# Kernel tuning notes

Hardware: AMD Instinct MI355X
Metric: run time of the kernel (lower is better)

Reference implementation:

```python
import jax, jax.numpy as jnp
import numpy as np
from jax import lax

DN = ('NCDHW', 'OIDHW', 'NCDHW')


def _ln(x, w, b, eps=1e-5):
    m = jnp.mean(x, -1, keepdims=True)
    v = jnp.mean((x - m) ** 2, -1, keepdims=True)
    return (x - m) * lax.rsqrt(v + eps) * w + b


def _gelu(x):
    return jax.nn.gelu(x, approximate=False)


def _dwconv3(v, w, b, groups):
    # depthwise 3x3x3, padding=1, stride=1; v:[B,C,H,W,D], w:[C,1,3,3,3]
    y = lax.conv_general_dilated(v, w, (1, 1, 1), 'SAME',
                                 dimension_numbers=DN,
                                 feature_group_count=groups)
    return y + b[None, :, None, None, None]


def _forward(x, ln1_w, ln1_b, q_w, sr1_w, sr1_b, n1_w, n1_b, sr2_w, sr2_b,
             n2_w, n2_b, kv1_w, kv2_w, lc1_w, lc1_b, lc2_w, lc2_b,
             proj_w, proj_b, ln2_w, ln2_b, fc1_w, fc1_b, fc2_w, fc2_b,
             H, W, D):
    B, N, C = x.shape
    h = 8
    h2 = h // 2
    hd = C // h
    scale = hd ** -0.5
    C2 = C // 2

    # ---- pre-norm + attention ----
    xa = _ln(x, ln1_w, ln1_b)
    q = (xa @ q_w.T).reshape(B, N, h, hd).transpose(0, 2, 1, 3)  # [B,h,N,hd]

    x_ = xa.transpose(0, 2, 1).reshape(B, C, H, W, D)
    # branch 1: conv k=2 s=2 spatial reduction
    y1 = lax.conv_general_dilated(x_, sr1_w, (2, 2, 2), 'VALID',
                                  dimension_numbers=DN) + sr1_b[None, :, None, None, None]
    N1 = (H // 2) * (W // 2) * (D // 2)
    x1 = _gelu(_ln(y1.reshape(B, C, N1).transpose(0, 2, 1), n1_w, n1_b))  # [B,N1,C]
    # branch 2: 1x1x1 conv, full resolution
    y2 = lax.conv_general_dilated(x_, sr2_w, (1, 1, 1), 'VALID',
                                  dimension_numbers=DN) + sr2_b[None, :, None, None, None]
    N2 = N
    x2 = _gelu(_ln(y2.reshape(B, C, N2).transpose(0, 2, 1), n2_w, n2_b))  # [B,N2,C]

    kv1 = (x1 @ kv1_w.T).reshape(B, N1, 2, h2, hd).transpose(2, 0, 3, 1, 4)
    k1, v1 = kv1[0], kv1[1]  # [B,h2,N1,hd]
    kv2 = (x2 @ kv2_w.T).reshape(B, N2, 2, h2, hd).transpose(2, 0, 3, 1, 4)
    k2, v2 = kv2[0], kv2[1]  # [B,h2,N2,hd]

    attn1 = jax.nn.softmax(jnp.einsum('bhnd,bhmd->bhnm', q[:, :h2], k1) * scale, axis=-1)
    v1sp = v1.transpose(0, 2, 1, 3).reshape(B, N1, C2).transpose(0, 2, 1).reshape(
        B, C2, H // 2, W // 2, D // 2)
    v1 = v1 + _dwconv3(v1sp, lc1_w, lc1_b, C2).reshape(B, h2, hd, N1).transpose(0, 1, 3, 2)
    o1 = jnp.einsum('bhnm,bhmd->bhnd', attn1, v1).transpose(0, 2, 1, 3).reshape(B, N, C2)

    attn2 = jax.nn.softmax(jnp.einsum('bhnd,bhmd->bhnm', q[:, h2:], k2) * scale, axis=-1)
    v2sp = v2.transpose(0, 2, 1, 3).reshape(B, N2, C2).transpose(0, 2, 1).reshape(B, C2, H, W, D)
    v2 = v2 + _dwconv3(v2sp, lc2_w, lc2_b, C2).reshape(B, h2, hd, N2).transpose(0, 1, 3, 2)
    o2 = jnp.einsum('bhnm,bhmd->bhnd', attn2, v2).transpose(0, 2, 1, 3).reshape(B, N, C2)

    att = jnp.concatenate([o1, o2], axis=-1) @ proj_w.T + proj_b
    x = x + att  # residual (drop_path = 0)

    # ---- pre-norm + MLP ----
    xm = _ln(x, ln2_w, ln2_b)
    mlp = _gelu(xm @ fc1_w.T + fc1_b) @ fc2_w.T + fc2_b
    return x + mlp


def setup_inputs() -> dict:
    key = jax.random.key(0)
    B, C, H, W, D = 2, 384, 16, 16, 16
    N = H * W * D
    hid = 4 * C
    C2 = C // 2
    ks = iter(jax.random.split(key, 32))
    rn = lambda shape, s=0.02: (jax.random.normal(next(ks), shape) * s).astype(jnp.float32)
    return {
        'x': jax.random.normal(next(ks), (B, N, C), jnp.float32),
        'ln1_w': jnp.ones(C, jnp.float32), 'ln1_b': jnp.zeros(C, jnp.float32),
        'q_w': rn((C, C)),
        'sr1_w': rn((C, C, 2, 2, 2), 0.025), 'sr1_b': jnp.zeros(C, jnp.float32),
        'n1_w': jnp.ones(C, jnp.float32), 'n1_b': jnp.zeros(C, jnp.float32),
        'sr2_w': rn((C, C, 1, 1, 1), 0.07), 'sr2_b': jnp.zeros(C, jnp.float32),
        'n2_w': jnp.ones(C, jnp.float32), 'n2_b': jnp.zeros(C, jnp.float32),
        'kv1_w': rn((C, C)), 'kv2_w': rn((C, C)),
        'lc1_w': rn((C2, 1, 3, 3, 3), 0.27), 'lc1_b': jnp.zeros(C2, jnp.float32),
        'lc2_w': rn((C2, 1, 3, 3, 3), 0.27), 'lc2_b': jnp.zeros(C2, jnp.float32),
        'proj_w': rn((C, C)), 'proj_b': jnp.zeros(C, jnp.float32),
        'ln2_w': jnp.ones(C, jnp.float32), 'ln2_b': jnp.zeros(C, jnp.float32),
        'fc1_w': rn((hid, C)), 'fc1_b': jnp.zeros(hid, jnp.float32),
        'fc2_w': rn((C, hid)), 'fc2_b': jnp.zeros(C, jnp.float32),
        'H': H, 'W': W, 'D': D,
    }


def reference(x, ln1_w, ln1_b, q_w, sr1_w, sr1_b, n1_w, n1_b, sr2_w, sr2_b,
              n2_w, n2_b, kv1_w, kv2_w, lc1_w, lc1_b, lc2_w, lc2_b,
              proj_w, proj_b, ln2_w, ln2_b, fc1_w, fc1_b, fc2_w, fc2_b,
              H, W, D):
    return _forward(x, ln1_w, ln1_b, q_w, sr1_w, sr1_b, n1_w, n1_b, sr2_w, sr2_b,
                    n2_w, n2_b, kv1_w, kv2_w, lc1_w, lc1_b, lc2_w, lc2_b,
                    proj_w, proj_b, ln2_w, ln2_b, fc1_w, fc1_b, fc2_w, fc2_b,
                    H, W, D)
```

## Files before the change

kernel.cpp:

```cpp
#include <hip/hip_runtime.h>

typedef unsigned short ushort_t;
typedef unsigned int uint_t;
typedef __bf16 bf16_t;
typedef __bf16 bf16x8 __attribute__((ext_vector_type(8)));
typedef float f32x4 __attribute__((ext_vector_type(4)));

__device__ __forceinline__ float b2f(ushort_t u) {
    union { uint_t i; float f; } v; v.i = ((uint_t)u) << 16; return v.f;
}
__device__ __forceinline__ ushort_t f2b(float f) {
    union { float f; uint_t i; } v; v.f = f;
    uint_t r = v.i + 0x7fffu + ((v.i >> 16) & 1u);
    return (ushort_t)(r >> 16);
}
__device__ __forceinline__ float gelu_exact(float x) {
    return 0.5f * x * (1.0f + erff(x * 0.70710678118654752f));
}

__global__ void prep_weights(const float* __restrict__ q_w, const float* __restrict__ sr2_w,
                             const float* __restrict__ kv1_w, const float* __restrict__ kv2_w,
                             const float* __restrict__ proj_w, const float* __restrict__ fc1_w,
                             const float* __restrict__ fc2_w, const float* __restrict__ sr1_w,
                             ushort_t* __restrict__ dst) {
    int gid = blockIdx.x * 256 + threadIdx.x;
    int i = gid;
    if (i < 147456) { dst[gid] = f2b(q_w[i]); return; }
    i -= 147456;
    if (i < 147456) { dst[gid] = f2b(sr2_w[i]); return; }
    i -= 147456;
    if (i < 147456) { dst[gid] = f2b(kv1_w[i]); return; }
    i -= 147456;
    if (i < 147456) { dst[gid] = f2b(kv2_w[i]); return; }
    i -= 147456;
    if (i < 147456) { dst[gid] = f2b(proj_w[i]); return; }
    i -= 147456;
    if (i < 589824) { dst[gid] = f2b(fc1_w[i]); return; }
    i -= 589824;
    if (i < 589824) { dst[gid] = f2b(fc2_w[i]); return; }
    i -= 589824;
    if (i < 1179648) {
        int co = i / 3072, r = i % 3072, kk = r / 384, ci = r % 384;
        dst[gid] = f2b(sr1_w[((size_t)co * 384 + ci) * 8 + kk]);
    }
}

__global__ void im2col_kernel(const ushort_t* __restrict__ xa, ushort_t* __restrict__ A1) {
    int gid = blockIdx.x * 256 + threadIdx.x;
    if (gid >= 1024 * 3072) return;
    int m = gid / 3072, r = gid % 3072, kk = r / 384, ci = r % 384;
    int b = m >> 9, n1 = m & 511;
    int ho = n1 >> 6, wo = (n1 >> 3) & 7, dz = n1 & 7;
    int n = ((2 * ho + ((kk >> 2) & 1)) << 8) + ((2 * wo + ((kk >> 1) & 1)) << 4) + (2 * dz + (kk & 1));
    A1[gid] = xa[((size_t)b * 4096 + n) * 384 + ci];
}

__global__ __launch_bounds__(128) void ln_kernel(const float* __restrict__ in,
                                                 const float* __restrict__ w,
                                                 const float* __restrict__ b,
                                                 float* __restrict__ outf,
                                                 ushort_t* __restrict__ outb, int act) {
    const int C = 384;
    int row = blockIdx.x, tid = threadIdx.x;
    size_t base = (size_t)row * C;
    float x[3], s = 0.f, s2 = 0.f;
#pragma unroll
    for (int i = 0; i < 3; i++) {
        int c = tid + i * 128;
        float v = in[base + c];
        x[i] = v; s += v; s2 += v * v;
    }
    for (int off = 32; off; off >>= 1) { s += __shfl_down(s, off); s2 += __shfl_down(s2, off); }
    __shared__ float sc[4];
    int lane = tid & 63, wid = tid >> 6;
    if (lane == 0) { sc[wid] = s; sc[wid + 2] = s2; }
    __syncthreads();
    float ts = sc[0] + sc[1], ts2 = sc[2] + sc[3];
    float mean = ts / C;
    float var = ts2 / C - mean * mean;
    float rstd = rsqrtf(var + 1e-5f);
#pragma unroll
    for (int i = 0; i < 3; i++) {
        int c = tid + i * 128;
        float v = (x[i] - mean) * rstd * w[c] + b[c];
        if (act) v = gelu_exact(v);
        if (outf) outf[base + c] = v;
        if (outb) outb[base + c] = f2b(v);
    }
}

__global__ __launch_bounds__(256) void mfma_gemm(const ushort_t* __restrict__ A,
                                                 const ushort_t* __restrict__ W,
                                                 const float* __restrict__ bias,
                                                 const float* __restrict__ res,
                                                 float* __restrict__ outf,
                                                 ushort_t* __restrict__ outb,
                                                 int M, int N, int K, int act) {
    __shared__ bf16_t Asl[128][40];
    __shared__ bf16_t Wsl[128][40];
    int tid = threadIdx.x;
    int wave = tid >> 6, lane = tid & 63, g = lane >> 4, c = lane & 15;
    int wm = wave >> 1, wn = wave & 1;
    int m0 = blockIdx.y * 128, n0 = blockIdx.x * 128;
    int srow = tid >> 1, sseg = tid & 1;

    f32x4 acc[4][4];
#pragma unroll
    for (int i = 0; i < 4; i++)
#pragma unroll
        for (int j = 0; j < 4; j++) acc[i][j] = f32x4{0.f, 0.f, 0.f, 0.f};

    for (int k0 = 0; k0 < K; k0 += 32) {
        const ushort_t* As = A + (size_t)(m0 + srow) * K + k0 + sseg * 16;
        const ushort_t* Ws = W + (size_t)(n0 + srow) * K + k0 + sseg * 16;
        uint4 av0 = *(const uint4*)As, av1 = *(const uint4*)(As + 8);
        uint4 wv0 = *(const uint4*)Ws, wv1 = *(const uint4*)(Ws + 8);
        __syncthreads();
        *(uint4*)&Asl[srow][sseg * 16] = av0;
        *(uint4*)&Asl[srow][sseg * 16 + 8] = av1;
        *(uint4*)&Wsl[srow][sseg * 16] = wv0;
        *(uint4*)&Wsl[srow][sseg * 16 + 8] = wv1;
        __syncthreads();
        bf16x8 af[4], bf[4];
#pragma unroll
        for (int fi = 0; fi < 4; fi++) af[fi] = *(bf16x8*)&Asl[wm * 64 + fi * 16 + c][g * 8];
#pragma unroll
        for (int fj = 0; fj < 4; fj++) bf[fj] = *(bf16x8*)&Wsl[wn * 64 + fj * 16 + c][g * 8];
#pragma unroll
        for (int fi = 0; fi < 4; fi++)
#pragma unroll
            for (int fj = 0; fj < 4; fj++)
                acc[fi][fj] = __builtin_amdgcn_mfma_f32_16x16x32_bf16(af[fi], bf[fj], acc[fi][fj], 0, 0, 0);
    }

#pragma unroll
    for (int fi = 0; fi < 4; fi++) {
#pragma unroll
        for (int fj = 0; fj < 4; fj++) {
            int n = n0 + wn * 64 + fj * 16 + c;
            float bv = bias ? bias[n] : 0.f;
#pragma unroll
            for (int i = 0; i < 4; i++) {
                int m = m0 + wm * 64 + fi * 16 + 4 * g + i;
                float v = acc[fi][fj][i] + bv;
                if (act == 1) v = gelu_exact(v);
                size_t idx = (size_t)m * N + n;
                if (res) v += res[idx];
                if (outf) outf[idx] = v;
                if (outb) outb[idx] = f2b(v);
            }
        }
    }
}

__global__ __launch_bounds__(256) void gemm64(const ushort_t* __restrict__ A,
                                              const ushort_t* __restrict__ W,
                                              const float* __restrict__ bias,
                                              const float* __restrict__ res,
                                              float* __restrict__ outf,
                                              ushort_t* __restrict__ outb,
                                              int M, int N, int K, int act, float oscale) {
    __shared__ bf16_t Asl[64][72];
    __shared__ bf16_t Wsl[64][72];
    int tid = threadIdx.x;
    int wave = tid >> 6, lane = tid & 63, g = lane >> 4, c = lane & 15;
    int wm = wave >> 1, wn = wave & 1;
    int m0 = blockIdx.y * 64, n0 = blockIdx.x * 64;
    int srow = tid >> 2, sseg = tid & 3;

    f32x4 acc[2][2];
#pragma unroll
    for (int i = 0; i < 2; i++)
#pragma unroll
        for (int j = 0; j < 2; j++) acc[i][j] = f32x4{0.f, 0.f, 0.f, 0.f};

    for (int k0 = 0; k0 < K; k0 += 64) {
        const ushort_t* As = A + (size_t)(m0 + srow) * K + k0 + sseg * 16;
        const ushort_t* Ws = W + (size_t)(n0 + srow) * K + k0 + sseg * 16;
        uint4 av0 = *(const uint4*)As, av1 = *(const uint4*)(As + 8);
        uint4 wv0 = *(const uint4*)Ws, wv1 = *(const uint4*)(Ws + 8);
        __syncthreads();
        *(uint4*)&Asl[srow][sseg * 16] = av0;
        *(uint4*)&Asl[srow][sseg * 16 + 8] = av1;
        *(uint4*)&Wsl[srow][sseg * 16] = wv0;
        *(uint4*)&Wsl[srow][sseg * 16 + 8] = wv1;
        __syncthreads();
#pragma unroll
        for (int kk = 0; kk < 2; kk++) {
            bf16x8 af[2], bf[2];
#pragma unroll
            for (int fi = 0; fi < 2; fi++) af[fi] = *(bf16x8*)&Asl[wm * 32 + fi * 16 + c][kk * 32 + g * 8];
#pragma unroll
            for (int fj = 0; fj < 2; fj++) bf[fj] = *(bf16x8*)&Wsl[wn * 32 + fj * 16 + c][kk * 32 + g * 8];
#pragma unroll
            for (int fi = 0; fi < 2; fi++)
#pragma unroll
                for (int fj = 0; fj < 2; fj++)
                    acc[fi][fj] = __builtin_amdgcn_mfma_f32_16x16x32_bf16(af[fi], bf[fj], acc[fi][fj], 0, 0, 0);
        }
    }

#pragma unroll
    for (int fi = 0; fi < 2; fi++) {
#pragma unroll
        for (int fj = 0; fj < 2; fj++) {
            int n = n0 + wn * 32 + fj * 16 + c;
            float bv = bias ? bias[n] : 0.f;
#pragma unroll
            for (int i = 0; i < 4; i++) {
                int m = m0 + wm * 32 + fi * 16 + 4 * g + i;
                float v = (acc[fi][fj][i] + bv) * oscale;
                if (act == 1) v = gelu_exact(v);
                size_t idx = (size_t)m * N + n;
                if (res) v += res[idx];
                if (outf) outf[idx] = v;
                if (outb) outb[idx] = f2b(v);
            }
        }
    }
}

__global__ __launch_bounds__(256) void gemm_qy2(const ushort_t* __restrict__ A,
                                                const ushort_t* __restrict__ W,
                                                const float* __restrict__ sr2_b,
                                                ushort_t* __restrict__ qb,
                                                float* __restrict__ y2f,
                                                int M, float qscale) {
    const int K = 384;
    __shared__ bf16_t Asl[64][72];
    __shared__ bf16_t Wsl[64][72];
    int tid = threadIdx.x;
    int wave = tid >> 6, lane = tid & 63, g = lane >> 4, c = lane & 15;
    int wm = wave >> 1, wn = wave & 1;
    int m0 = blockIdx.y * 64, n0 = blockIdx.x * 64;
    int srow = tid >> 2, sseg = tid & 3;

    f32x4 acc[2][2];
#pragma unroll
    for (int i = 0; i < 2; i++)
#pragma unroll
        for (int j = 0; j < 2; j++) acc[i][j] = f32x4{0.f, 0.f, 0.f, 0.f};

    for (int k0 = 0; k0 < K; k0 += 64) {
        const ushort_t* As = A + (size_t)(m0 + srow) * K + k0 + sseg * 16;
        const ushort_t* Ws = W + (size_t)(n0 + srow) * K + k0 + sseg * 16;
        uint4 av0 = *(const uint4*)As, av1 = *(const uint4*)(As + 8);
        uint4 wv0 = *(const uint4*)Ws, wv1 = *(const uint4*)(Ws + 8);
        __syncthreads();
        *(uint4*)&Asl[srow][sseg * 16] = av0;
        *(uint4*)&Asl[srow][sseg * 16 + 8] = av1;
        *(uint4*)&Wsl[srow][sseg * 16] = wv0;
        *(uint4*)&Wsl[srow][sseg * 16 + 8] = wv1;
        __syncthreads();
#pragma unroll
        for (int kk = 0; kk < 2; kk++) {
            bf16x8 af[2], bf[2];
#pragma unroll
            for (int fi = 0; fi < 2; fi++) af[fi] = *(bf16x8*)&Asl[wm * 32 + fi * 16 + c][kk * 32 + g * 8];
#pragma unroll
            for (int fj = 0; fj < 2; fj++) bf[fj] = *(bf16x8*)&Wsl[wn * 32 + fj * 16 + c][kk * 32 + g * 8];
#pragma unroll
            for (int fi = 0; fi < 2; fi++)
#pragma unroll
                for (int fj = 0; fj < 2; fj++)
                    acc[fi][fj] = __builtin_amdgcn_mfma_f32_16x16x32_bf16(af[fi], bf[fj], acc[fi][fj], 0, 0, 0);
        }
    }

    int isq = (n0 < 384);
#pragma unroll
    for (int fi = 0; fi < 2; fi++) {
#pragma unroll
        for (int fj = 0; fj < 2; fj++) {
            int n = n0 + wn * 32 + fj * 16 + c;
#pragma unroll
            for (int i = 0; i < 4; i++) {
                int m = m0 + wm * 32 + fi * 16 + 4 * g + i;
                float v = acc[fi][fj][i];
                if (isq) {
                    qb[(size_t)m * 384 + n] = f2b(v * qscale);
                } else {
                    y2f[(size_t)m * 384 + (n - 384)] = v + sr2_b[n - 384];
                }
            }
        }
    }
}

__global__ void dwconv_kernel(const ushort_t* __restrict__ vin,
                              const float* __restrict__ wt,
                              const float* __restrict__ bias,
                              ushort_t* __restrict__ vout,
                              int Hs, int Wsz, int Ds, int S, int total) {
    int gid = blockIdx.x * 256 + threadIdx.x;
    if (gid >= total) return;
    int c2 = gid % 192;
    int r = gid / 192;
    int n = r % S;
    int b = r / S;
    int dz = n % Ds, wy = (n / Ds) % Wsz, hx = n / (Wsz * Ds);
    float center = b2f(vin[(size_t)(b * S + n) * 384 + c2]);
    float acc = bias[c2];
    for (int kh = -1; kh <= 1; kh++) {
        int h2 = hx + kh; if (h2 < 0 || h2 >= Hs) continue;
        for (int kw = -1; kw <= 1; kw++) {
            int w2 = wy + kw; if (w2 < 0 || w2 >= Wsz) continue;
            for (int kd = -1; kd <= 1; kd++) {
                int d2 = dz + kd; if (d2 < 0 || d2 >= Ds) continue;
                int nn = (h2 * Wsz + w2) * Ds + d2;
                acc += b2f(vin[(size_t)(b * S + nn) * 384 + c2]) *
                       wt[c2 * 27 + (kh + 1) * 9 + (kw + 1) * 3 + (kd + 1)];
            }
        }
    }
    vout[(size_t)(b * S + n) * 192 + c2] = f2b(center + acc);
}

__global__ __launch_bounds__(256) void transpose_kernel(const ushort_t* __restrict__ src,
                                                        ushort_t* __restrict__ dst, int S) {
    __shared__ ushort_t t_lds[64][65];
    int n0 = blockIdx.x * 64, c0 = blockIdx.y * 64, b = blockIdx.z;
    int tid = threadIdx.x;
#pragma unroll
    for (int i = 0; i < 16; i++) {
        int idx = tid + i * 256;
        int r = idx >> 6, cc = idx & 63;
        t_lds[r][cc] = src[((size_t)b * S + n0 + r) * 192 + c0 + cc];
    }
    __syncthreads();
#pragma unroll
    for (int i = 0; i < 16; i++) {
        int idx = tid + i * 256;
        int r = idx >> 6, cc = idx & 63;
        dst[((size_t)b * 192 + c0 + r) * S + n0 + cc] = t_lds[cc][r];
    }
}

__global__ __launch_bounds__(256, 4) void attn_mfma5(
    const ushort_t* __restrict__ qbuf,
    const ushort_t* __restrict__ kv1,
    const ushort_t* __restrict__ kv2,
    const ushort_t* __restrict__ vt1,
    const ushort_t* __restrict__ vt2,
    ushort_t* __restrict__ obuf)
{
    __shared__ __align__(16) char lds_raw[18432];
    bf16_t (*P)[32][72] = (bf16_t (*)[32][72])lds_raw;
    float (*CF)[64][14] = (float (*)[64][14])lds_raw;

    const int N = 4096;
    int tid = threadIdx.x;
    int q0 = blockIdx.x * 32, hl = 7 - blockIdx.y, b = blockIdx.z;
    int wave = tid >> 6, lane = tid & 63, g = lane >> 4, c = lane & 15;
    int br2 = hl >> 2;
    int NK = br2 ? 4096 : 512;
    const ushort_t* kbuf = br2 ? kv2 : kv1;
    const ushort_t* vtb  = br2 ? vt2 : vt1;
    int hloc = hl & 3;
    int NKc = NK >> 2;
    int kb0 = wave * NKc;
    int nkt = NKc >> 6;

    union { uint4 u; bf16x8 v; } zz; zz.u = uint4{0u, 0u, 0u, 0u};
    const bf16x8 zero8 = zz.v;

    bf16x8 bq0[2], bq1[2];
#pragma unroll
    for (int qg = 0; qg < 2; qg++) {
        const ushort_t* qrowp = qbuf + ((size_t)b * N + q0 + qg * 16 + c) * 384 + hl * 48;
        bq0[qg] = *(const bf16x8*)(qrowp + g * 8);
        bq1[qg] = (g < 2) ? *(const bf16x8*)(qrowp + 32 + g * 8) : zero8;
    }

    f32x4 of[3][2];
#pragma unroll
    for (int dt = 0; dt < 3; dt++)
#pragma unroll
        for (int qg = 0; qg < 2; qg++) of[dt][qg] = f32x4{0.f, 0.f, 0.f, 0.f};
    float l_acc[2] = {0.f, 0.f};

    const ushort_t* kp = kbuf + ((size_t)b * NK + kb0 + c) * 384 + hloc * 48;
    const ushort_t* vp = vtb + ((size_t)b * 192 + hloc * 48 + c) * NK + kb0;

    for (int kt = 0; kt < nkt; kt++) {
        f32x4 sf[4][2];
#pragma unroll
        for (int t = 0; t < 4; t++)
#pragma unroll
            for (int qg = 0; qg < 2; qg++) sf[t][qg] = f32x4{0.f, 0.f, 0.f, 0.f};
#pragma unroll
        for (int t = 0; t < 4; t++) {
            const ushort_t* kr = kp + (size_t)(kt * 64 + 16 * t) * 384;
            bf16x8 ak0 = *(const bf16x8*)(kr + g * 8);
            bf16x8 ak1 = (g < 2) ? *(const bf16x8*)(kr + 32 + g * 8) : zero8;
#pragma unroll
            for (int qg = 0; qg < 2; qg++) {
                sf[t][qg] = __builtin_amdgcn_mfma_f32_16x16x32_bf16(ak0, bq0[qg], sf[t][qg], 0, 0, 0);
                sf[t][qg] = __builtin_amdgcn_mfma_f32_16x16x32_bf16(ak1, bq1[qg], sf[t][qg], 0, 0, 0);
            }
        }

#pragma unroll
        for (int qg = 0; qg < 2; qg++) {
#pragma unroll
            for (int t = 0; t < 4; t++) {
                union { ushort4 v; bf16_t h[4]; } pk;
#pragma unroll
                for (int i = 0; i < 4; i++) {
                    float p = exp2f(sf[t][qg][i]);
                    l_acc[qg] += p;
                    pk.h[i] = (bf16_t)p;
                }
                *(ushort4*)&P[wave][qg * 16 + c][16 * t + 4 * g] = pk.v;
            }
        }

        asm volatile("s_waitcnt lgkmcnt(0)" ::: "memory");

        bf16x8 pb0[2], pb1[2];
#pragma unroll
        for (int qg = 0; qg < 2; qg++) {
            pb0[qg] = *(bf16x8*)&P[wave][qg * 16 + c][g * 8];
            pb1[qg] = *(bf16x8*)&P[wave][qg * 16 + c][32 + g * 8];
        }
#pragma unroll
        for (int dt = 0; dt < 3; dt++) {
            const ushort_t* vr = vp + (size_t)(16 * dt) * NK + kt * 64;
            bf16x8 av0 = *(const bf16x8*)(vr + g * 8);
            bf16x8 av1 = *(const bf16x8*)(vr + 32 + g * 8);
#pragma unroll
            for (int qg = 0; qg < 2; qg++) {
                of[dt][qg] = __builtin_amdgcn_mfma_f32_16x16x32_bf16(av0, pb0[qg], of[dt][qg], 0, 0, 0);
                of[dt][qg] = __builtin_amdgcn_mfma_f32_16x16x32_bf16(av1, pb1[qg], of[dt][qg], 0, 0, 0);
            }
        }
    }

#pragma unroll
    for (int qg = 0; qg < 2; qg++) {
        l_acc[qg] += __shfl_xor(l_acc[qg], 16);
        l_acc[qg] += __shfl_xor(l_acc[qg], 32);
    }

#pragma unroll
    for (int qg = 0; qg < 2; qg++) {
        __syncthreads();
        float* cfp = &CF[wave][lane][0];
#pragma unroll
        for (int dt = 0; dt < 3; dt++)
#pragma unroll
            for (int i = 0; i < 4; i++) cfp[dt * 4 + i] = of[dt][qg][i];
        cfp[12] = l_acc[qg];
        __syncthreads();
        if (wave == 0) {
            float lsum = 0.f;
            float oc[12];
#pragma unroll
            for (int j = 0; j < 12; j++) oc[j] = 0.f;
#pragma unroll
            for (int w = 0; w < 4; w++) {
                lsum += CF[w][lane][12];
#pragma unroll
                for (int j = 0; j < 12; j++) oc[j] += CF[w][lane][j];
            }
            float rl = 1.f / lsum;
            int qrow = q0 + qg * 16 + c;
#pragma unroll
            for (int dt = 0; dt < 3; dt++) {
                union { ushort4 v; bf16_t h[4]; } pk;
#pragma unroll
                for (int i = 0; i < 4; i++) pk.h[i] = (bf16_t)(oc[dt * 4 + i] * rl);
                *(ushort4*)&obuf[((size_t)b * N + qrow) * 384 + hl * 48 + 16 * dt + 4 * g] = pk.v;
            }
        }
    }
}

extern "C" void kernel_launch(void* const* d_in, const int* in_sizes, int n_in,
                              void* d_out, int out_size, void* d_ws, size_t ws_size,
                              hipStream_t stream) {
    const int B = 2, N = 4096, C = 384, N1 = 512, HID = 1536;
    const float* x      = (const float*)d_in[0];
    const float* ln1_w  = (const float*)d_in[1];
    const float* ln1_b  = (const float*)d_in[2];
    const float* q_w    = (const float*)d_in[3];
    const float* sr1_w  = (const float*)d_in[4];
    const float* sr1_b  = (const float*)d_in[5];
    const float* n1_w   = (const float*)d_in[6];
    const float* n1_b   = (const float*)d_in[7];
    const float* sr2_w  = (const float*)d_in[8];
    const float* sr2_b  = (const float*)d_in[9];
    const float* n2_w   = (const float*)d_in[10];
    const float* n2_b   = (const float*)d_in[11];
    const float* kv1_w  = (const float*)d_in[12];
    const float* kv2_w  = (const float*)d_in[13];
    const float* lc1_w  = (const float*)d_in[14];
    const float* lc1_b  = (const float*)d_in[15];
    const float* lc2_w  = (const float*)d_in[16];
    const float* lc2_b  = (const float*)d_in[17];
    const float* proj_w = (const float*)d_in[18];
    const float* proj_b = (const float*)d_in[19];
    const float* ln2_w  = (const float*)d_in[20];
    const float* ln2_b  = (const float*)d_in[21];
    const float* fc1_w  = (const float*)d_in[22];
    const float* fc1_b  = (const float*)d_in[23];
    const float* fc2_w  = (const float*)d_in[24];
    const float* fc2_b  = (const float*)d_in[25];
    float* out = (float*)d_out;

    char* ws = (char*)d_ws;
    ushort_t* wbase = (ushort_t*)ws;
    ushort_t* wqy2 = wbase;
    ushort_t* wkv1 = wbase + 294912;
    ushort_t* wkv2 = wbase + 442368;
    ushort_t* wproj= wbase + 589824;
    ushort_t* wfc1 = wbase + 737280;
    ushort_t* wfc2 = wbase + 1327104;
    ushort_t* wsr1 = wbase + 1916928;
    ushort_t* xa_bf = (ushort_t*)(ws + 6193152);
    ushort_t* qbB   = (ushort_t*)(ws + 12484608);
    ushort_t* x2_bf = (ushort_t*)(ws + 18776064);
    ushort_t* kv2   = (ushort_t*)(ws + 25067520);
    ushort_t* vmod2 = (ushort_t*)(ws + 31358976);
    ushort_t* kv1   = (ushort_t*)(ws + 34504704);
    ushort_t* vmod1 = (ushort_t*)(ws + 35291136);
    ushort_t* x1_bf = (ushort_t*)(ws + 35684352);
    float*    y2f   = (float*)(ws + 36470784);
    float*    y1f   = (float*)(ws + 49053696);
    ushort_t* A1    = (ushort_t*)(ws + 50626560);
    ushort_t* hid   = (ushort_t*)(ws + 56918016);
    ushort_t* vt2   = (ushort_t*)(ws + 82083840);
    ushort_t* vt1   = (ushort_t*)(ws + 85229568);
    ushort_t* Obuf  = xa_bf;
    float*    xres  = y2f;
    ushort_t* xm_bf = A1;

    const float QSCALE = 0.14433756729740643f * 1.4426950408889634f;

    prep_weights<<<(3096576 + 255) / 256, 256, 0, stream>>>(q_w, sr2_w, kv1_w, kv2_w,
                                                            proj_w, fc1_w, fc2_w, sr1_w, wbase);
    ln_kernel<<<B * N, 128, 0, stream>>>(x, ln1_w, ln1_b, nullptr, xa_bf, 0);
    gemm_qy2<<<dim3(12, 128), 256, 0, stream>>>(xa_bf, wqy2, sr2_b, qbB, y2f, B * N, QSCALE);
    ln_kernel<<<B * N, 128, 0, stream>>>(y2f, n2_w, n2_b, nullptr, x2_bf, 1);
    im2col_kernel<<<(1024 * 3072 + 255) / 256, 256, 0, stream>>>(xa_bf, A1);
    gemm64<<<dim3(6, 16), 256, 0, stream>>>(A1, wsr1, sr1_b, nullptr,
                                            y1f, nullptr, 1024, C, 3072, 0, 1.f);
    ln_kernel<<<B * N1, 128, 0, stream>>>(y1f, n1_w, n1_b, nullptr, x1_bf, 1);
    gemm64<<<dim3(6, 128), 256, 0, stream>>>(x2_bf, wkv2, nullptr, nullptr,
                                             nullptr, kv2, B * N, C, C, 0, 1.f);
    gemm64<<<dim3(6, 16), 256, 0, stream>>>(x1_bf, wkv1, nullptr, nullptr,
                                            nullptr, kv1, 1024, C, C, 0, 1.f);
    {
        int total2 = B * N * 192;
        dwconv_kernel<<<(total2 + 255) / 256, 256, 0, stream>>>(kv2 + 192, lc2_w, lc2_b, vmod2,
                                                                16, 16, 16, N, total2);
        int total1 = B * N1 * 192;
        dwconv_kernel<<<(total1 + 255) / 256, 256, 0, stream>>>(kv1 + 192, lc1_w, lc1_b, vmod1,
                                                                8, 8, 8, N1, total1);
        transpose_kernel<<<dim3(64, 3, 2), 256, 0, stream>>>(vmod2, vt2, 4096);
        transpose_kernel<<<dim3(8, 3, 2), 256, 0, stream>>>(vmod1, vt1, 512);
    }
    attn_mfma5<<<dim3(N / 32, 8, B), 256, 0, stream>>>(qbB, kv1, kv2, vt1, vt2, Obuf);
    gemm64<<<dim3(6, 128), 256, 0, stream>>>(Obuf, wproj, proj_b, x,
                                             xres, nullptr, B * N, C, C, 0, 1.f);
    ln_kernel<<<B * N, 128, 0, stream>>>(xres, ln2_w, ln2_b, nullptr, xm_bf, 0);
    mfma_gemm<<<dim3(12, 64), 256, 0, stream>>>(xm_bf, wfc1, fc1_b, nullptr,
                                                nullptr, hid, B * N, HID, C, 1);
    gemm64<<<dim3(6, 128), 256, 0, stream>>>(hid, wfc2, fc2_b, xres,
                                             out, nullptr, B * N, C, HID, 0, 1.f);
}
```

Before: 346.0 us.

## Prefetch next K-tile in GEMMs, merge dwconv/transpose launches, hoist V loads

```diff
diff --git a/kernel.cpp b/kernel.cpp
--- a/kernel.cpp
+++ b/kernel.cpp
@@ -103,6 +103,8 @@
     int wm = wave >> 1, wn = wave & 1;
     int m0 = blockIdx.y * 128, n0 = blockIdx.x * 128;
     int srow = tid >> 1, sseg = tid & 1;
+    const ushort_t* Abase = A + (size_t)(m0 + srow) * K + sseg * 16;
+    const ushort_t* Wbase = W + (size_t)(n0 + srow) * K + sseg * 16;
 
     f32x4 acc[4][4];
 #pragma unroll
@@ -110,17 +112,23 @@
 #pragma unroll
         for (int j = 0; j < 4; j++) acc[i][j] = f32x4{0.f, 0.f, 0.f, 0.f};
 
+    uint4 av0 = *(const uint4*)Abase, av1 = *(const uint4*)(Abase + 8);
+    uint4 wv0 = *(const uint4*)Wbase, wv1 = *(const uint4*)(Wbase + 8);
     for (int k0 = 0; k0 < K; k0 += 32) {
-        const ushort_t* As = A + (size_t)(m0 + srow) * K + k0 + sseg * 16;
-        const ushort_t* Ws = W + (size_t)(n0 + srow) * K + k0 + sseg * 16;
-        uint4 av0 = *(const uint4*)As, av1 = *(const uint4*)(As + 8);
-        uint4 wv0 = *(const uint4*)Ws, wv1 = *(const uint4*)(Ws + 8);
         __syncthreads();
         *(uint4*)&Asl[srow][sseg * 16] = av0;
         *(uint4*)&Asl[srow][sseg * 16 + 8] = av1;
         *(uint4*)&Wsl[srow][sseg * 16] = wv0;
         *(uint4*)&Wsl[srow][sseg * 16 + 8] = wv1;
         __syncthreads();
+        uint4 nav0, nav1, nwv0, nwv1;
+        bool more = (k0 + 32 < K);
+        if (more) {
+            nav0 = *(const uint4*)(Abase + k0 + 32);
+            nav1 = *(const uint4*)(Abase + k0 + 40);
+            nwv0 = *(const uint4*)(Wbase + k0 + 32);
+            nwv1 = *(const uint4*)(Wbase + k0 + 40);
+        }
         bf16x8 af[4], bf[4];
 #pragma unroll
         for (int fi = 0; fi < 4; fi++) af[fi] = *(bf16x8*)&Asl[wm * 64 + fi * 16 + c][g * 8];
@@ -131,6 +139,7 @@
 #pragma unroll
             for (int fj = 0; fj < 4; fj++)
                 acc[fi][fj] = __builtin_amdgcn_mfma_f32_16x16x32_bf16(af[fi], bf[fj], acc[fi][fj], 0, 0, 0);
+        if (more) { av0 = nav0; av1 = nav1; wv0 = nwv0; wv1 = nwv1; }
     }
 
 #pragma unroll
@@ -167,6 +176,8 @@
     int wm = wave >> 1, wn = wave & 1;
     int m0 = blockIdx.y * 64, n0 = blockIdx.x * 64;
     int srow = tid >> 2, sseg = tid & 3;
+    const ushort_t* Abase = A + (size_t)(m0 + srow) * K + sseg * 16;
+    const ushort_t* Wbase = W + (size_t)(n0 + srow) * K + sseg * 16;
 
     f32x4 acc[2][2];
 #pragma unroll
@@ -174,17 +185,23 @@
 #pragma unroll
         for (int j = 0; j < 2; j++) acc[i][j] = f32x4{0.f, 0.f, 0.f, 0.f};
 
+    uint4 av0 = *(const uint4*)Abase, av1 = *(const uint4*)(Abase + 8);
+    uint4 wv0 = *(const uint4*)Wbase, wv1 = *(const uint4*)(Wbase + 8);
     for (int k0 = 0; k0 < K; k0 += 64) {
-        const ushort_t* As = A + (size_t)(m0 + srow) * K + k0 + sseg * 16;
-        const ushort_t* Ws = W + (size_t)(n0 + srow) * K + k0 + sseg * 16;
-        uint4 av0 = *(const uint4*)As, av1 = *(const uint4*)(As + 8);
-        uint4 wv0 = *(const uint4*)Ws, wv1 = *(const uint4*)(Ws + 8);
         __syncthreads();
         *(uint4*)&Asl[srow][sseg * 16] = av0;
         *(uint4*)&Asl[srow][sseg * 16 + 8] = av1;
         *(uint4*)&Wsl[srow][sseg * 16] = wv0;
         *(uint4*)&Wsl[srow][sseg * 16 + 8] = wv1;
         __syncthreads();
+        uint4 nav0, nav1, nwv0, nwv1;
+        bool more = (k0 + 64 < K);
+        if (more) {
+            nav0 = *(const uint4*)(Abase + k0 + 64);
+            nav1 = *(const uint4*)(Abase + k0 + 72);
+            nwv0 = *(const uint4*)(Wbase + k0 + 64);
+            nwv1 = *(const uint4*)(Wbase + k0 + 72);
+        }
 #pragma unroll
         for (int kk = 0; kk < 2; kk++) {
             bf16x8 af[2], bf[2];
@@ -198,6 +215,7 @@
                 for (int fj = 0; fj < 2; fj++)
                     acc[fi][fj] = __builtin_amdgcn_mfma_f32_16x16x32_bf16(af[fi], bf[fj], acc[fi][fj], 0, 0, 0);
         }
+        if (more) { av0 = nav0; av1 = nav1; wv0 = nwv0; wv1 = nwv1; }
     }
 
 #pragma unroll
@@ -234,6 +252,8 @@
     int wm = wave >> 1, wn = wave & 1;
     int m0 = blockIdx.y * 64, n0 = blockIdx.x * 64;
     int srow = tid >> 2, sseg = tid & 3;
+    const ushort_t* Abase = A + (size_t)(m0 + srow) * K + sseg * 16;
+    const ushort_t* Wbase = W + (size_t)(n0 + srow) * K + sseg * 16;
 
     f32x4 acc[2][2];
 #pragma unroll
@@ -241,17 +261,23 @@
 #pragma unroll
         for (int j = 0; j < 2; j++) acc[i][j] = f32x4{0.f, 0.f, 0.f, 0.f};
 
+    uint4 av0 = *(const uint4*)Abase, av1 = *(const uint4*)(Abase + 8);
+    uint4 wv0 = *(const uint4*)Wbase, wv1 = *(const uint4*)(Wbase + 8);
     for (int k0 = 0; k0 < K; k0 += 64) {
-        const ushort_t* As = A + (size_t)(m0 + srow) * K + k0 + sseg * 16;
-        const ushort_t* Ws = W + (size_t)(n0 + srow) * K + k0 + sseg * 16;
-        uint4 av0 = *(const uint4*)As, av1 = *(const uint4*)(As + 8);
-        uint4 wv0 = *(const uint4*)Ws, wv1 = *(const uint4*)(Ws + 8);
         __syncthreads();
         *(uint4*)&Asl[srow][sseg * 16] = av0;
         *(uint4*)&Asl[srow][sseg * 16 + 8] = av1;
         *(uint4*)&Wsl[srow][sseg * 16] = wv0;
         *(uint4*)&Wsl[srow][sseg * 16 + 8] = wv1;
         __syncthreads();
+        uint4 nav0, nav1, nwv0, nwv1;
+        bool more = (k0 + 64 < K);
+        if (more) {
+            nav0 = *(const uint4*)(Abase + k0 + 64);
+            nav1 = *(const uint4*)(Abase + k0 + 72);
+            nwv0 = *(const uint4*)(Wbase + k0 + 64);
+            nwv1 = *(const uint4*)(Wbase + k0 + 72);
+        }
 #pragma unroll
         for (int kk = 0; kk < 2; kk++) {
             bf16x8 af[2], bf[2];
@@ -265,6 +291,7 @@
                 for (int fj = 0; fj < 2; fj++)
                     acc[fi][fj] = __builtin_amdgcn_mfma_f32_16x16x32_bf16(af[fi], bf[fj], acc[fi][fj], 0, 0, 0);
         }
+        if (more) { av0 = nav0; av1 = nav1; wv0 = nwv0; wv1 = nwv1; }
     }
 
     int isq = (n0 < 384);
@@ -287,13 +314,11 @@
     }
 }
 
-__global__ void dwconv_kernel(const ushort_t* __restrict__ vin,
-                              const float* __restrict__ wt,
-                              const float* __restrict__ bias,
-                              ushort_t* __restrict__ vout,
-                              int Hs, int Wsz, int Ds, int S, int total) {
-    int gid = blockIdx.x * 256 + threadIdx.x;
-    if (gid >= total) return;
+__device__ __forceinline__ void dwconv_one(const ushort_t* __restrict__ vin,
+                                           const float* __restrict__ wt,
+                                           const float* __restrict__ bias,
+                                           ushort_t* __restrict__ vout,
+                                           int Hs, int Wsz, int Ds, int S, int gid) {
     int c2 = gid % 192;
     int r = gid / 192;
     int n = r % S;
@@ -316,10 +341,27 @@
     vout[(size_t)(b * S + n) * 192 + c2] = f2b(center + acc);
 }
 
-__global__ __launch_bounds__(256) void transpose_kernel(const ushort_t* __restrict__ src,
-                                                        ushort_t* __restrict__ dst, int S) {
+__global__ void dwconv2_kernel(const ushort_t* __restrict__ v2in, const ushort_t* __restrict__ v1in,
+                               const float* __restrict__ w2, const float* __restrict__ b2,
+                               const float* __restrict__ w1, const float* __restrict__ b1,
+                               ushort_t* __restrict__ vo2, ushort_t* __restrict__ vo1) {
+    int gid = blockIdx.x * 256 + threadIdx.x;
+    const int T2 = 2 * 4096 * 192;
+    const int T1 = 2 * 512 * 192;
+    if (gid < T2) dwconv_one(v2in, w2, b2, vo2, 16, 16, 16, 4096, gid);
+    else if (gid < T2 + T1) dwconv_one(v1in, w1, b1, vo1, 8, 8, 8, 512, gid - T2);
+}
+
+__global__ __launch_bounds__(256) void transpose2_kernel(const ushort_t* __restrict__ src2,
+                                                         ushort_t* __restrict__ dst2,
+                                                         const ushort_t* __restrict__ src1,
+                                                         ushort_t* __restrict__ dst1) {
     __shared__ ushort_t t_lds[64][65];
-    int n0 = blockIdx.x * 64, c0 = blockIdx.y * 64, b = blockIdx.z;
+    int bx = blockIdx.x;
+    const ushort_t* src; ushort_t* dst; int S, n0;
+    if (bx < 64) { src = src2; dst = dst2; S = 4096; n0 = bx * 64; }
+    else         { src = src1; dst = dst1; S = 512;  n0 = (bx - 64) * 64; }
+    int c0 = blockIdx.y * 64, b = blockIdx.z;
     int tid = threadIdx.x;
 #pragma unroll
     for (int i = 0; i < 16; i++) {
@@ -336,7 +378,7 @@
     }
 }
 
-__global__ __launch_bounds__(256, 4) void attn_mfma5(
+__global__ __launch_bounds__(256, 4) void attn_mfma7(
     const ushort_t* __restrict__ qbuf,
     const ushort_t* __restrict__ kv1,
     const ushort_t* __restrict__ kv2,
@@ -383,6 +425,14 @@
     const ushort_t* vp = vtb + ((size_t)b * 192 + hloc * 48 + c) * NK + kb0;
 
     for (int kt = 0; kt < nkt; kt++) {
+        bf16x8 av0[3], av1[3];
+#pragma unroll
+        for (int dt = 0; dt < 3; dt++) {
+            const ushort_t* vr = vp + (size_t)(16 * dt) * NK + kt * 64;
+            av0[dt] = *(const bf16x8*)(vr + g * 8);
+            av1[dt] = *(const bf16x8*)(vr + 32 + g * 8);
+        }
+
         f32x4 sf[4][2];
 #pragma unroll
         for (int t = 0; t < 4; t++)
@@ -425,13 +475,10 @@
         }
 #pragma unroll
         for (int dt = 0; dt < 3; dt++) {
-            const ushort_t* vr = vp + (size_t)(16 * dt) * NK + kt * 64;
-            bf16x8 av0 = *(const bf16x8*)(vr + g * 8);
-            bf16x8 av1 = *(const bf16x8*)(vr + 32 + g * 8);
 #pragma unroll
             for (int qg = 0; qg < 2; qg++) {
-                of[dt][qg] = __builtin_amdgcn_mfma_f32_16x16x32_bf16(av0, pb0[qg], of[dt][qg], 0, 0, 0);
-                of[dt][qg] = __builtin_amdgcn_mfma_f32_16x16x32_bf16(av1, pb1[qg], of[dt][qg], 0, 0, 0);
+                of[dt][qg] = __builtin_amdgcn_mfma_f32_16x16x32_bf16(av0[dt], pb0[qg], of[dt][qg], 0, 0, 0);
+                of[dt][qg] = __builtin_amdgcn_mfma_f32_16x16x32_bf16(av1[dt], pb1[qg], of[dt][qg], 0, 0, 0);
             }
         }
     }
@@ -551,16 +598,13 @@
     gemm64<<<dim3(6, 16), 256, 0, stream>>>(x1_bf, wkv1, nullptr, nullptr,
                                             nullptr, kv1, 1024, C, C, 0, 1.f);
     {
-        int total2 = B * N * 192;
-        dwconv_kernel<<<(total2 + 255) / 256, 256, 0, stream>>>(kv2 + 192, lc2_w, lc2_b, vmod2,
-                                                                16, 16, 16, N, total2);
-        int total1 = B * N1 * 192;
-        dwconv_kernel<<<(total1 + 255) / 256, 256, 0, stream>>>(kv1 + 192, lc1_w, lc1_b, vmod1,
-                                                                8, 8, 8, N1, total1);
-        transpose_kernel<<<dim3(64, 3, 2), 256, 0, stream>>>(vmod2, vt2, 4096);
-        transpose_kernel<<<dim3(8, 3, 2), 256, 0, stream>>>(vmod1, vt1, 512);
-    }
-    attn_mfma5<<<dim3(N / 32, 8, B), 256, 0, stream>>>(qbB, kv1, kv2, vt1, vt2, Obuf);
+        const int T2 = B * N * 192, T1 = B * N1 * 192;
+        dwconv2_kernel<<<(T2 + T1 + 255) / 256, 256, 0, stream>>>(kv2 + 192, kv1 + 192,
+                                                                  lc2_w, lc2_b, lc1_w, lc1_b,
+                                                                  vmod2, vmod1);
+        transpose2_kernel<<<dim3(72, 3, 2), 256, 0, stream>>>(vmod2, vt2, vmod1, vt1);
+    }
+    attn_mfma7<<<dim3(N / 32, 8, B), 256, 0, stream>>>(qbB, kv1, kv2, vt1, vt2, Obuf);
     gemm64<<<dim3(6, 128), 256, 0, stream>>>(Obuf, wproj, proj_b, x,
                                              xres, nullptr, B * N, C, C, 0, 1.f);
     ln_kernel<<<B * N, 128, 0, stream>>>(xres, ln2_w, ln2_b, nullptr, xm_bf, 0);
```

After: 342.3 us. No clear change (-1.1%).
